# Kernel optimization log

Measured on AMD Instinct MI355X. Metric: run time of the kernel, lower is better.

The kernel has to match this reference:

```python
import jax, jax.numpy as jnp
import numpy as np

N = 50000       # num_entities / nodes
E = 100000      # edges
K = 8           # incoming edge-graph neighbors per edge
D_NODE = 64
D_EDGE = 64
H = 4
DH = D_EDGE // H
DIN = D_EDGE + 2 * D_NODE  # [edge_feat, node_feat[src], node_feat[dst]]


def setup_inputs() -> dict:
    key = jax.random.key(0)
    ks = jax.random.split(key, 6)
    node_features = jax.random.normal(ks[0], (N, D_NODE), jnp.float32)
    edge_features = jax.random.normal(ks[1], (E, D_EDGE), jnp.float32)
    edge_index = jax.random.randint(ks[2], (2, E), 0, N)
    node_tiers = jax.random.randint(ks[3], (N,), 0, 4, dtype=jnp.int32)
    # edge adjacency (line graph): each edge attends to K other edges
    adj_dst = jnp.repeat(jnp.arange(E), K)                       # [A]
    adj_src = jax.random.randint(ks[4], (E * K,), 0, E)          # [A]
    # learned params: two EdgeAttention layers, each Wq/Wk/Wv [DIN,D_EDGE], Wo [D_EDGE,D_EDGE]
    wkeys = jax.random.split(ks[5], 8)
    def w(k, fan_in, fan_out):
        return jax.random.normal(k, (fan_in, fan_out), jnp.float32) * np.float32(1.0 / np.sqrt(fan_in))
    params = {}
    for li in (1, 2):
        base = (li - 1) * 4
        params[f'l{li}_Wq'] = w(wkeys[base + 0], DIN, D_EDGE)
        params[f'l{li}_Wk'] = w(wkeys[base + 1], DIN, D_EDGE)
        params[f'l{li}_Wv'] = w(wkeys[base + 2], DIN, D_EDGE)
        params[f'l{li}_Wo'] = w(wkeys[base + 3], D_EDGE, D_EDGE)
    return dict(node_features=node_features, edge_features=edge_features,
                edge_index=edge_index, node_tiers=node_tiers,
                adj_src=adj_src, adj_dst=adj_dst, **params)


def _edge_attention(node_f, edge_f, edge_index, adj_src, adj_dst, Wq, Wk, Wv, Wo):
    # x: edge feature conditioned on endpoint node features  [E, DIN]
    x = jnp.concatenate([edge_f, node_f[edge_index[0]], node_f[edge_index[1]]], axis=-1)
    q = (x @ Wq).reshape(E, H, DH)
    k = (x @ Wk).reshape(E, H, DH)
    v = (x @ Wv).reshape(E, H, DH)
    scale = np.float32(1.0 / np.sqrt(DH))
    # scores per adjacency pair  [A, H]
    s = jnp.einsum('ahd,ahd->ah', q[adj_dst], k[adj_src]) * scale
    # segment softmax over incoming neighbors of each dst edge
    m = jax.ops.segment_max(s, adj_dst, num_segments=E)          # [E, H]
    e = jnp.exp(s - m[adj_dst])                                   # [A, H]
    denom = jax.ops.segment_sum(e, adj_dst, num_segments=E)      # [E, H]
    alpha = e / denom[adj_dst]                                    # [A, H]
    out = jax.ops.segment_sum(alpha[..., None] * v[adj_src], adj_dst, num_segments=E)  # [E,H,DH]
    return edge_f + out.reshape(E, D_EDGE) @ Wo                   # residual


def reference(node_features, edge_features, edge_index, node_tiers, adj_src, adj_dst,
              l1_Wq, l1_Wk, l1_Wv, l1_Wo, l2_Wq, l2_Wk, l2_Wv, l2_Wo):
    ef = _edge_attention(node_features, edge_features, edge_index, adj_src, adj_dst,
                         l1_Wq, l1_Wk, l1_Wv, l1_Wo)
    ef = _edge_attention(node_features, ef, edge_index, adj_src, adj_dst,
                         l2_Wq, l2_Wk, l2_Wv, l2_Wo)
    return ef  # updated edge features of the output DeltaGraph
```

## Files before the change

### kernel.cpp

```cpp
#include <hip/hip_runtime.h>

#define NE 100000
#define NN 50000

typedef short short8 __attribute__((ext_vector_type(8)));
typedef float f32x4 __attribute__((ext_vector_type(4)));
typedef unsigned short ushort;
typedef unsigned int uint;

__device__ inline ushort f2bf(float f) {
    unsigned int u = __float_as_uint(f);
    u += 0x7FFFu + ((u >> 16) & 1u);
    return (ushort)(u >> 16);
}
__device__ inline float bf2f(ushort u) {
    return __uint_as_float((unsigned int)u << 16);
}

__device__ inline short8 pack_bf8(float4 a, float4 b) {
    short8 r;
    r[0] = (short)f2bf(a.x); r[1] = (short)f2bf(a.y);
    r[2] = (short)f2bf(a.z); r[3] = (short)f2bf(a.w);
    r[4] = (short)f2bf(b.x); r[5] = (short)f2bf(b.y);
    r[6] = (short)f2bf(b.z); r[7] = (short)f2bf(b.w);
    return r;
}

__global__ __launch_bounds__(256) void prep_qkv_w(
    const float* __restrict__ Wq, const float* __restrict__ Wk,
    const float* __restrict__ Wv, ushort* __restrict__ wf)
{
    int idx = blockIdx.x * 256 + threadIdx.x;
    if (idx >= 6 * 12 * 64) return;
    int lane = idx & 63;
    int st = idx >> 6;
    int s = st / 12, t = st % 12;
    int n = t * 16 + (lane & 15);
    int kb = s * 32 + (lane >> 4) * 8;
    const float* w = (n < 64) ? Wq : (n < 128) ? Wk : Wv;
    int nn = n & 63;
    #pragma unroll
    for (int j = 0; j < 8; ++j)
        wf[(size_t)idx * 8 + j] = f2bf(w[(size_t)(kb + j) * 64 + nn]);
}

__global__ __launch_bounds__(256) void prep_wo_w(
    const float* __restrict__ Wo, ushort* __restrict__ wf)
{
    int idx = blockIdx.x * 256 + threadIdx.x;
    if (idx >= 2 * 4 * 64) return;
    int lane = idx & 63;
    int st = idx >> 6;
    int s = st / 4, t = st % 4;
    int n = t * 16 + (lane & 15);
    int kb = s * 32 + (lane >> 4) * 8;
    #pragma unroll
    for (int j = 0; j < 8; ++j)
        wf[(size_t)idx * 8 + j] = f2bf(Wo[(size_t)(kb + j) * 64 + n]);
}

__global__ __launch_bounds__(256, 3) void qkv_mfma(
    const float* __restrict__ ef, const float* __restrict__ nodef,
    const int* __restrict__ eidx, const ushort* __restrict__ wfrag,
    ushort* __restrict__ qo, ushort* __restrict__ ko, ushort* __restrict__ vo)
{
    __shared__ __align__(16) char lds_a[24 * 1056];

    const int tid = threadIdx.x;
    const int l   = tid & 63;
    const int w   = tid >> 6;

    short8 Bf[6][3];
    #pragma unroll
    for (int s = 0; s < 6; ++s)
        #pragma unroll
        for (int n = 0; n < 3; ++n)
            Bf[s][n] = *(const short8*)((const char*)wfrag +
                        (size_t)((s * 12 + 3 * w + n) * 64 + l) * 16);

    {
        const int r64 = tid >> 2;
        const int p   = tid & 3;
        const int row = blockIdx.x * 64 + r64;
        const int rc  = (row < NE) ? row : NE - 1;
        const float* srcs[3] = { ef    + (size_t)rc * 64,
                                 nodef + (size_t)eidx[rc] * 64,
                                 nodef + (size_t)eidx[NE + rc] * 64 };
        #pragma unroll
        for (int c = 0; c < 3; ++c) {
            const float* sp = srcs[c] + p * 16;
            float4 f0 = *(const float4*)(sp + 0);
            float4 f1 = *(const float4*)(sp + 4);
            float4 f2 = *(const float4*)(sp + 8);
            float4 f3 = *(const float4*)(sp + 12);
            short8 lo = pack_bf8(f0, f1);
            short8 hi = pack_bf8(f2, f3);
            const int regbase = (w * 3 + c) * 2;
            *(short8*)(lds_a + (size_t)(regbase + 0) * 1056 + l * 16) = lo;
            *(short8*)(lds_a + (size_t)(regbase + 1) * 1056 + l * 16) = hi;
        }
    }

    f32x4 acc[4][3];
    #pragma unroll
    for (int T = 0; T < 4; ++T)
        #pragma unroll
        for (int n = 0; n < 3; ++n) acc[T][n] = (f32x4)(0.f);

    __syncthreads();

    const int r  = l & 15;
    const int kg = l >> 4;
    #pragma unroll
    for (int s = 0; s < 6; ++s) {
        short8 Af[4];
        #pragma unroll
        for (int T = 0; T < 4; ++T) {
            const int region = (T * 3 + (s >> 1)) * 2 + (kg & 1);
            const int slot   = r * 4 + (s & 1) * 2 + (kg >> 1);
            Af[T] = *(const short8*)(lds_a + (size_t)region * 1056 + slot * 16);
        }
        #pragma unroll
        for (int T = 0; T < 4; ++T)
            #pragma unroll
            for (int n = 0; n < 3; ++n)
                acc[T][n] = __builtin_amdgcn_mfma_f32_16x16x32_bf16(
                                Af[T], Bf[s][n], acc[T][n], 0, 0, 0);
    }

    const int e0 = blockIdx.x * 64;
    #pragma unroll
    for (int T = 0; T < 4; ++T) {
        #pragma unroll
        for (int n = 0; n < 3; ++n) {
            const int c = (3 * w + n) * 16 + r;
            ushort* dst = (c < 64) ? (qo + c) : (c < 128) ? (ko + (c - 64))
                                              : (vo + (c - 128));
            #pragma unroll
            for (int jj = 0; jj < 4; ++jj) {
                const int row = e0 + T * 16 + kg * 4 + jj;
                if (row < NE) dst[(size_t)row * 64] = f2bf(acc[T][n][jj]);
            }
        }
    }
}

__global__ __launch_bounds__(256) void attn_kernel(
    const ushort* __restrict__ q, const ushort* __restrict__ kbuf,
    const ushort* __restrict__ vbuf, const int* __restrict__ adj_src,
    ushort* __restrict__ ao)
{
    const int wid  = (blockIdx.x * 256 + threadIdx.x) >> 6;
    const int lane = threadIdx.x & 63;
    if (wid >= NE) return;
    const int e    = wid;
    const int half = lane >> 5;
    const int l32  = lane & 31;

    ushort2 qu = *(const ushort2*)(q + (size_t)e * 64 + l32 * 2);
    const float q0 = bf2f(qu.x), q1 = bf2f(qu.y);

    int nbr[4];
    float s[4];
    #pragma unroll
    for (int t = 0; t < 4; ++t) {
        nbr[t] = adj_src[e * 8 + 2 * t + half];
        ushort2 ku = *(const ushort2*)(kbuf + (size_t)nbr[t] * 64 + l32 * 2);
        float p = q0 * bf2f(ku.x) + q1 * bf2f(ku.y);
        p += __shfl_xor(p, 1);
        p += __shfl_xor(p, 2);
        p += __shfl_xor(p, 4);
        s[t] = p * 0.25f;
    }

    float m = fmaxf(fmaxf(s[0], s[1]), fmaxf(s[2], s[3]));
    m = fmaxf(m, __shfl_xor(m, 32));
    float w[4], den = 0.f;
    #pragma unroll
    for (int t = 0; t < 4; ++t) { w[t] = __expf(s[t] - m); den += w[t]; }
    den += __shfl_xor(den, 32);
    const float inv = 1.f / den;

    float ox = 0.f, oy = 0.f;
    #pragma unroll
    for (int t = 0; t < 4; ++t) {
        ushort2 vu = *(const ushort2*)(vbuf + (size_t)nbr[t] * 64 + l32 * 2);
        ox = fmaf(w[t], bf2f(vu.x), ox);
        oy = fmaf(w[t], bf2f(vu.y), oy);
    }
    ox = (ox + __shfl_xor(ox, 32)) * inv;
    oy = (oy + __shfl_xor(oy, 32)) * inv;

    if (lane < 32) {
        ushort2 o;
        o.x = f2bf(ox);
        o.y = f2bf(oy);
        *(ushort2*)(ao + (size_t)e * 64 + l32 * 2) = o;
    }
}

__global__ __launch_bounds__(256) void wo_mfma(
    const float* __restrict__ ef_in, const ushort* __restrict__ attn,
    const ushort* __restrict__ wofrag, float* __restrict__ efo)
{
    const int wave = threadIdx.x >> 6;
    const int lane = threadIdx.x & 63;
    const int r  = lane & 15;
    const int kg = lane >> 4;
    const int e0 = blockIdx.x * 64 + wave * 16;
    const int e  = e0 + r;
    const int ec = (e < NE) ? e : NE - 1;

    short8 afr[2];
    #pragma unroll
    for (int s = 0; s < 2; ++s)
        afr[s] = *(const short8*)(attn + (size_t)ec * 64 + s * 32 + kg * 8);

    const short8* wf = (const short8*)wofrag;
    f32x4 acc[4];
    #pragma unroll
    for (int t = 0; t < 4; ++t) acc[t] = (f32x4)(0.f);
    #pragma unroll
    for (int s = 0; s < 2; ++s) {
        #pragma unroll
        for (int t = 0; t < 4; ++t) {
            short8 b = wf[(size_t)(s * 4 + t) * 64 + lane];
            acc[t] = __builtin_amdgcn_mfma_f32_16x16x32_bf16(afr[s], b, acc[t], 0, 0, 0);
        }
    }

    const int orow = e0 + kg * 4;
    #pragma unroll
    for (int t = 0; t < 4; ++t) {
        const int c = t * 16 + r;
        #pragma unroll
        for (int j = 0; j < 4; ++j) {
            int row = orow + j;
            if (row < NE) {
                size_t off = (size_t)row * 64 + c;
                efo[off] = acc[t][j] + ef_in[off];
            }
        }
    }
}

extern "C" void kernel_launch(void* const* d_in, const int* in_sizes, int n_in,
                              void* d_out, int out_size, void* d_ws, size_t ws_size,
                              hipStream_t stream)
{
    const float* nodef   = (const float*)d_in[0];
    const float* ef      = (const float*)d_in[1];
    const int*   eidx    = (const int*)d_in[2];
    const int*   adj_src = (const int*)d_in[4];
    const float* l1Wq = (const float*)d_in[6];
    const float* l1Wk = (const float*)d_in[7];
    const float* l1Wv = (const float*)d_in[8];
    const float* l1Wo = (const float*)d_in[9];
    const float* l2Wq = (const float*)d_in[10];
    const float* l2Wk = (const float*)d_in[11];
    const float* l2Wv = (const float*)d_in[12];
    const float* l2Wo = (const float*)d_in[13];

    ushort* q  = (ushort*)d_ws;
    ushort* k  = q  + (size_t)NE * 64;
    ushort* v  = k  + (size_t)NE * 64;
    ushort* ao = v  + (size_t)NE * 64;
    ushort* wf1 = ao + (size_t)NE * 64;
    ushort* wf2 = wf1 + 36864;
    ushort* wo1 = wf2 + 36864;
    ushort* wo2 = wo1 + 4096;
    float* out = (float*)d_out;

    dim3 blk(256);
    const int gq = (NE + 63) / 64;
    const int ga = (NE + 3) / 4;
    const int gw = (NE + 63) / 64;

    prep_qkv_w<<<18, blk, 0, stream>>>(l1Wq, l1Wk, l1Wv, wf1);
    prep_qkv_w<<<18, blk, 0, stream>>>(l2Wq, l2Wk, l2Wv, wf2);
    prep_wo_w<<<2, blk, 0, stream>>>(l1Wo, wo1);
    prep_wo_w<<<2, blk, 0, stream>>>(l2Wo, wo2);

    qkv_mfma<<<gq, blk, 0, stream>>>(ef, nodef, eidx, wf1, q, k, v);
    attn_kernel<<<ga, blk, 0, stream>>>(q, k, v, adj_src, ao);
    wo_mfma<<<gw, blk, 0, stream>>>(ef, ao, wo1, out);
    qkv_mfma<<<gq, blk, 0, stream>>>(out, nodef, eidx, wf2, q, k, v);
    attn_kernel<<<ga, blk, 0, stream>>>(q, k, v, adj_src, ao);
    wo_mfma<<<gw, blk, 0, stream>>>(out, ao, wo2, out);
}
```

Measured before the change: 148.6 us.

## Fuse weight-prep launches, halve QKV tile rows, batch attention gathers

The four weight-packing kernels are merged into one launch to cut launch overhead. The QKV MFMA kernel now processes 32 rows per block with a padded row-major LDS layout, doubling the grid for better occupancy and load balance, at the cost of reloading the B fragments into registers for each block. The attention kernel loads the neighbor indices with one int4 load and issues all K and V gathers up front, so more memory requests are in flight at once.

```diff
diff --git a/kernel.cpp b/kernel.cpp
--- a/kernel.cpp
+++ b/kernel.cpp
@@ -26,14 +26,11 @@
     return r;
 }
 
-__global__ __launch_bounds__(256) void prep_qkv_w(
-    const float* __restrict__ Wq, const float* __restrict__ Wk,
-    const float* __restrict__ Wv, ushort* __restrict__ wf)
-{
-    int idx = blockIdx.x * 256 + threadIdx.x;
-    if (idx >= 6 * 12 * 64) return;
-    int lane = idx & 63;
-    int st = idx >> 6;
+__device__ inline void pack_qkv_slot(int slot, const float* Wq, const float* Wk,
+                                     const float* Wv, ushort* wf)
+{
+    int lane = slot & 63;
+    int st = slot >> 6;
     int s = st / 12, t = st % 12;
     int n = t * 16 + (lane & 15);
     int kb = s * 32 + (lane >> 4) * 8;
@@ -41,22 +38,34 @@
     int nn = n & 63;
     #pragma unroll
     for (int j = 0; j < 8; ++j)
-        wf[(size_t)idx * 8 + j] = f2bf(w[(size_t)(kb + j) * 64 + nn]);
-}
-
-__global__ __launch_bounds__(256) void prep_wo_w(
-    const float* __restrict__ Wo, ushort* __restrict__ wf)
-{
-    int idx = blockIdx.x * 256 + threadIdx.x;
-    if (idx >= 2 * 4 * 64) return;
-    int lane = idx & 63;
-    int st = idx >> 6;
+        wf[(size_t)slot * 8 + j] = f2bf(w[(size_t)(kb + j) * 64 + nn]);
+}
+
+__device__ inline void pack_wo_slot(int slot, const float* Wo, ushort* wf)
+{
+    int lane = slot & 63;
+    int st = slot >> 6;
     int s = st / 4, t = st % 4;
     int n = t * 16 + (lane & 15);
     int kb = s * 32 + (lane >> 4) * 8;
     #pragma unroll
     for (int j = 0; j < 8; ++j)
-        wf[(size_t)idx * 8 + j] = f2bf(Wo[(size_t)(kb + j) * 64 + n]);
+        wf[(size_t)slot * 8 + j] = f2bf(Wo[(size_t)(kb + j) * 64 + n]);
+}
+
+__global__ __launch_bounds__(256) void prep_all(
+    const float* __restrict__ l1Wq, const float* __restrict__ l1Wk,
+    const float* __restrict__ l1Wv, const float* __restrict__ l1Wo,
+    const float* __restrict__ l2Wq, const float* __restrict__ l2Wk,
+    const float* __restrict__ l2Wv, const float* __restrict__ l2Wo,
+    ushort* __restrict__ wf1, ushort* __restrict__ wf2,
+    ushort* __restrict__ wo1, ushort* __restrict__ wo2)
+{
+    int idx = blockIdx.x * 256 + threadIdx.x;
+    if (idx < 4608)            pack_qkv_slot(idx,         l1Wq, l1Wk, l1Wv, wf1);
+    else if (idx < 9216)       pack_qkv_slot(idx - 4608,  l2Wq, l2Wk, l2Wv, wf2);
+    else if (idx < 9728)       pack_wo_slot (idx - 9216,  l1Wo, wo1);
+    else if (idx < 10240)      pack_wo_slot (idx - 9728,  l2Wo, wo2);
 }
 
 __global__ __launch_bounds__(256, 3) void qkv_mfma(
@@ -64,7 +73,7 @@
     const int* __restrict__ eidx, const ushort* __restrict__ wfrag,
     ushort* __restrict__ qo, ushort* __restrict__ ko, ushort* __restrict__ vo)
 {
-    __shared__ __align__(16) char lds_a[24 * 1056];
+    __shared__ __align__(16) ushort lds_a[32 * 200];
 
     const int tid = threadIdx.x;
     const int l   = tid & 63;
@@ -79,61 +88,52 @@
                         (size_t)((s * 12 + 3 * w + n) * 64 + l) * 16);
 
     {
-        const int r64 = tid >> 2;
-        const int p   = tid & 3;
-        const int row = blockIdx.x * 64 + r64;
+        const int r   = tid >> 3;
+        const int p   = tid & 7;
+        const int row = blockIdx.x * 32 + r;
         const int rc  = (row < NE) ? row : NE - 1;
         const float* srcs[3] = { ef    + (size_t)rc * 64,
                                  nodef + (size_t)eidx[rc] * 64,
                                  nodef + (size_t)eidx[NE + rc] * 64 };
         #pragma unroll
         for (int c = 0; c < 3; ++c) {
-            const float* sp = srcs[c] + p * 16;
+            const float* sp = srcs[c] + p * 8;
             float4 f0 = *(const float4*)(sp + 0);
             float4 f1 = *(const float4*)(sp + 4);
-            float4 f2 = *(const float4*)(sp + 8);
-            float4 f3 = *(const float4*)(sp + 12);
-            short8 lo = pack_bf8(f0, f1);
-            short8 hi = pack_bf8(f2, f3);
-            const int regbase = (w * 3 + c) * 2;
-            *(short8*)(lds_a + (size_t)(regbase + 0) * 1056 + l * 16) = lo;
-            *(short8*)(lds_a + (size_t)(regbase + 1) * 1056 + l * 16) = hi;
-        }
-    }
-
-    f32x4 acc[4][3];
-    #pragma unroll
-    for (int T = 0; T < 4; ++T)
+            *(short8*)(lds_a + r * 200 + c * 64 + p * 8) = pack_bf8(f0, f1);
+        }
+    }
+
+    f32x4 acc[2][3];
+    #pragma unroll
+    for (int T = 0; T < 2; ++T)
         #pragma unroll
         for (int n = 0; n < 3; ++n) acc[T][n] = (f32x4)(0.f);
 
     __syncthreads();
 
-    const int r  = l & 15;
+    const int rr = l & 15;
     const int kg = l >> 4;
     #pragma unroll
     for (int s = 0; s < 6; ++s) {
-        short8 Af[4];
-        #pragma unroll
-        for (int T = 0; T < 4; ++T) {
-            const int region = (T * 3 + (s >> 1)) * 2 + (kg & 1);
-            const int slot   = r * 4 + (s & 1) * 2 + (kg >> 1);
-            Af[T] = *(const short8*)(lds_a + (size_t)region * 1056 + slot * 16);
-        }
-        #pragma unroll
-        for (int T = 0; T < 4; ++T)
+        short8 Af[2];
+        #pragma unroll
+        for (int T = 0; T < 2; ++T)
+            Af[T] = *(const short8*)(lds_a + (T * 16 + rr) * 200 + s * 32 + kg * 8);
+        #pragma unroll
+        for (int T = 0; T < 2; ++T)
             #pragma unroll
             for (int n = 0; n < 3; ++n)
                 acc[T][n] = __builtin_amdgcn_mfma_f32_16x16x32_bf16(
                                 Af[T], Bf[s][n], acc[T][n], 0, 0, 0);
     }
 
-    const int e0 = blockIdx.x * 64;
-    #pragma unroll
-    for (int T = 0; T < 4; ++T) {
+    const int e0 = blockIdx.x * 32;
+    #pragma unroll
+    for (int T = 0; T < 2; ++T) {
         #pragma unroll
         for (int n = 0; n < 3; ++n) {
-            const int c = (3 * w + n) * 16 + r;
+            const int c = (3 * w + n) * 16 + rr;
             ushort* dst = (c < 64) ? (qo + c) : (c < 128) ? (ko + (c - 64))
                                               : (vo + (c - 128));
             #pragma unroll
@@ -157,16 +157,23 @@
     const int half = lane >> 5;
     const int l32  = lane & 31;
 
+    const int4 nb = *(const int4*)(adj_src + e * 8 + half * 4);
+    const int nbr[4] = { nb.x, nb.y, nb.z, nb.w };
+
     ushort2 qu = *(const ushort2*)(q + (size_t)e * 64 + l32 * 2);
     const float q0 = bf2f(qu.x), q1 = bf2f(qu.y);
 
-    int nbr[4];
+    ushort2 ku[4], vu[4];
+    #pragma unroll
+    for (int t = 0; t < 4; ++t) {
+        ku[t] = *(const ushort2*)(kbuf + (size_t)nbr[t] * 64 + l32 * 2);
+        vu[t] = *(const ushort2*)(vbuf + (size_t)nbr[t] * 64 + l32 * 2);
+    }
+
     float s[4];
     #pragma unroll
     for (int t = 0; t < 4; ++t) {
-        nbr[t] = adj_src[e * 8 + 2 * t + half];
-        ushort2 ku = *(const ushort2*)(kbuf + (size_t)nbr[t] * 64 + l32 * 2);
-        float p = q0 * bf2f(ku.x) + q1 * bf2f(ku.y);
+        float p = q0 * bf2f(ku[t].x) + q1 * bf2f(ku[t].y);
         p += __shfl_xor(p, 1);
         p += __shfl_xor(p, 2);
         p += __shfl_xor(p, 4);
@@ -175,18 +182,17 @@
 
     float m = fmaxf(fmaxf(s[0], s[1]), fmaxf(s[2], s[3]));
     m = fmaxf(m, __shfl_xor(m, 32));
-    float w[4], den = 0.f;
-    #pragma unroll
-    for (int t = 0; t < 4; ++t) { w[t] = __expf(s[t] - m); den += w[t]; }
+    float wgt[4], den = 0.f;
+    #pragma unroll
+    for (int t = 0; t < 4; ++t) { wgt[t] = __expf(s[t] - m); den += wgt[t]; }
     den += __shfl_xor(den, 32);
     const float inv = 1.f / den;
 
     float ox = 0.f, oy = 0.f;
     #pragma unroll
     for (int t = 0; t < 4; ++t) {
-        ushort2 vu = *(const ushort2*)(vbuf + (size_t)nbr[t] * 64 + l32 * 2);
-        ox = fmaf(w[t], bf2f(vu.x), ox);
-        oy = fmaf(w[t], bf2f(vu.y), oy);
+        ox = fmaf(wgt[t], bf2f(vu[t].x), ox);
+        oy = fmaf(wgt[t], bf2f(vu[t].y), oy);
     }
     ox = (ox + __shfl_xor(ox, 32)) * inv;
     oy = (oy + __shfl_xor(oy, 32)) * inv;
@@ -272,14 +278,13 @@
     float* out = (float*)d_out;
 
     dim3 blk(256);
-    const int gq = (NE + 63) / 64;
+    const int gq = (NE + 31) / 32;
     const int ga = (NE + 3) / 4;
     const int gw = (NE + 63) / 64;
 
-    prep_qkv_w<<<18, blk, 0, stream>>>(l1Wq, l1Wk, l1Wv, wf1);
-    prep_qkv_w<<<18, blk, 0, stream>>>(l2Wq, l2Wk, l2Wv, wf2);
-    prep_wo_w<<<2, blk, 0, stream>>>(l1Wo, wo1);
-    prep_wo_w<<<2, blk, 0, stream>>>(l2Wo, wo2);
+    prep_all<<<40, blk, 0, stream>>>(l1Wq, l1Wk, l1Wv, l1Wo,
+                                     l2Wq, l2Wk, l2Wv, l2Wo,
+                                     wf1, wf2, wo1, wo2);
 
     qkv_mfma<<<gq, blk, 0, stream>>>(ef, nodef, eidx, wf1, q, k, v);
     attn_kernel<<<ga, blk, 0, stream>>>(q, k, v, adj_src, ao);
```

Measured after the change: 142.3 us. -4.3%, faster.
